# Kernel tuning notes

Measured on AMD Instinct MI355X. Metric: run time of the kernel, lower is better.

The kernel has to match this reference:

```python
import jax, jax.numpy as jnp
import numpy as np

HID = 512      # hidden_dim
SEQ = 784      # sequence length hard-coded via make_discrete_HiPPO_nojit(hidden, 784)
BATCH = 1024
OUT = 10


def make_discrete_hippo(N, L):
    # HiPPO-LegS continuous matrices (standard construction)
    n = np.arange(N, dtype=np.float64)
    P = np.sqrt(1.0 + 2.0 * n)
    A = P[:, None] * P[None, :]
    A = -(np.tril(A) - np.diag(n))          # (N, N)
    B = np.sqrt(2.0 * n + 1.0).reshape(N, 1)  # (N, 1)
    # bilinear (Tustin) discretization with step = 1/L
    step = 1.0 / L
    I = np.eye(N)
    BL = np.linalg.inv(I - (step / 2.0) * A)
    Ad = BL @ (I + (step / 2.0) * A)
    Bd = (BL * step) @ B
    return jnp.asarray(Ad, jnp.float32), jnp.asarray(Bd[:, 0], jnp.float32)


def setup_inputs() -> dict:
    key = jax.random.key(0)
    k1, k2, k3, k4 = jax.random.split(key, 4)
    x = jax.random.normal(k1, (BATCH, SEQ), jnp.float32)
    # xavier-uniform C params (flax nn.initializers.xavier_uniform)
    a0 = float(np.sqrt(6.0 / (1 + HID)))
    a1 = float(np.sqrt(6.0 / (HID + HID)))
    C0 = jax.random.uniform(k2, (1, HID), jnp.float32, -a0, a0)
    C1 = jax.random.uniform(k3, (HID, HID), jnp.float32, -a1, a1)
    # final Dense(output_dim): lecun_normal kernel, zero bias
    W = jax.random.normal(k4, (HID, OUT), jnp.float32) / np.sqrt(HID)
    b = jnp.zeros((OUT,), jnp.float32)
    return {"x": x, "C0": C0, "C1": C1, "W": W, "b": b}


def _ssm_layer(A, Bvec, C, u):
    # u: (batch, seq) scalar input per step; returns ys: (seq, batch, d_out)
    def step(h, u_t):  # h: (batch, HID), u_t: (batch,)
        h_next = jnp.tanh(h @ A.T + u_t[:, None] * Bvec[None, :])
        y = h_next @ C.T
        return h_next, y
    h0 = jnp.zeros((u.shape[0], HID), u.dtype)
    _, ys = jax.lax.scan(step, h0, u.T)
    return ys


def reference(x, C0, C1, W, b):
    A, Bvec = make_discrete_hippo(HID, SEQ)  # trace-time constants
    y0 = _ssm_layer(A, Bvec, C0, x)[:, :, 0].T   # (batch, seq) scalar stream
    y1 = _ssm_layer(A, Bvec, C1, y0)             # (seq, batch, HID)
    logits = y1[-1] @ W + b                      # last timestep -> Dense
    return logits
```

## Files before the change

kernel.cpp:

```cpp
#include <hip/hip_runtime.h>
#include <math.h>

#define SEQL 784
#define HIDN 512
#define OUTD 10

typedef float v2 __attribute__((ext_vector_type(2)));

template<int CTRL, int RM>
__device__ __forceinline__ float dpp0(float v) {
    int r = __builtin_amdgcn_update_dpp(0, __builtin_bit_cast(int, v),
                                        CTRL, RM, 0xF, true);
    return __builtin_bit_cast(float, r);
}
__device__ __forceinline__ v2 sp(float v) { v2 r; r.x = v; r.y = v; return r; }
__device__ __forceinline__ v2 vfma(v2 a, v2 b, v2 c) {
    return __builtin_elementwise_fma(a, b, c);
}

__global__ __launch_bounds__(256) void compute_M(const float* __restrict__ C1,
                                                 const float* __restrict__ W,
                                                 float* __restrict__ M) {
    __shared__ float Ws[HIDN * OUTD];
    __shared__ float red[4][64][OUTD];
    const int lane = threadIdx.x & 63, w = threadIdx.x >> 6;
    const int i = blockIdx.x * 64 + lane;
    for (int idx = threadIdx.x; idx < HIDN * OUTD; idx += 256) Ws[idx] = W[idx];
    __syncthreads();
    float acc[OUTD];
#pragma unroll
    for (int o = 0; o < OUTD; ++o) acc[o] = 0.f;
    for (int j = w * 128; j < w * 128 + 128; ++j) {
        float cv = C1[j * HIDN + i];
#pragma unroll
        for (int o = 0; o < OUTD; ++o) acc[o] = fmaf(cv, Ws[j * OUTD + o], acc[o]);
    }
#pragma unroll
    for (int o = 0; o < OUTD; ++o) red[w][lane][o] = acc[o];
    __syncthreads();
    if (w == 0) {
#pragma unroll
        for (int o = 0; o < OUTD; ++o)
            M[i * OUTD + o] = (red[0][lane][o] + red[1][lane][o]) +
                              (red[2][lane][o] + red[3][lane][o]);
    }
}

__global__ __launch_bounds__(256, 1) void ssm_main(const float* __restrict__ x,
                                                   const float* __restrict__ C0,
                                                   const float* __restrict__ Mmat,
                                                   const float* __restrict__ bias,
                                                   float* __restrict__ out) {
    const int tid = threadIdx.x;
    const int wave = tid >> 6;
    const int lane = tid & 63;
    const int row = blockIdx.x * 4 + wave;

    __shared__ __align__(16) float xs[4][SEQL + 8];

    const float DEL = 1.0f / 784.0f;
    {
        const float4* __restrict__ xv =
            (const float4*)(x + (size_t)blockIdx.x * 4 * SEQL);
#pragma unroll
        for (int it = 0; it < 4; ++it) {
            int idx = tid + it * 256;
            if (idx < SEQL) {
                float4 v = xv[idx];
                int r = idx / (SEQL / 4);
                int c = (idx % (SEQL / 4)) * 4;
                float4 w;
                w.x = DEL * v.x; w.y = DEL * v.y;
                w.z = DEL * v.z; w.w = DEL * v.w;
                *(float4*)&xs[r][c] = w;
            }
        }
    }
    if (tid < 32) xs[tid >> 3][SEQL + (tid & 7)] = 0.f;
    __syncthreads();

    const double cd = 1.0 / 1568.0;
    const double F = 2.0 * 1.4426950408889634;
    float P[8], Ps[8], a_[8], G2[8], mE2[8], FT[8], C0d[8], K_[8];
    double apD = 0.0, bpD = 1.0;
    double Aprod = 1.0;
#pragma unroll
    for (int j = 0; j < 8; ++j) {
        int i = lane * 8 + j;
        double Pd = sqrt(1.0 + 2.0 * (double)i);
        double dd = 1.0 + cd * (double)(i + 1);
        double fd = 1.0 / dd;
        double ad = (1.0 - cd * (double)i) * fd;
        double mEd = -cd * Pd * fd;
        double ed = Pd * mEd;
        double Gd = (1.0 - cd * (double)(i + 1)) * fd;
        apD = ad * apD + ed;
        bpD = ad * bpD;
        P[j]   = (float)Pd;
        Ps[j]  = (float)(Pd / F);
        a_[j]  = (float)ad;
        G2[j]  = (float)(F * Gd);
        mE2[j] = (float)(F * mEd);
        FT[j]  = (float)(F * Pd * fd);
        K_[j]  = (float)(F * mEd * Aprod);
        Aprod *= ad;
        C0d[j] = DEL * C0[i];
    }
    float ac[6], bc[6];
    {
        double al = apD, be = bpD;
        int rl = lane & 15;
#pragma unroll
        for (int L = 0; L < 4; ++L) {
            int d = 1 << L;
            ac[L] = (float)al; bc[L] = (float)be;
            double pa = __shfl_up(al, d, 64);
            double pb = __shfl_up(be, d, 64);
            if (rl >= d) { al += be * pa; be *= pb; }
        }
        ac[4] = (float)al; bc[4] = (float)be;
        {
            int src = (lane & 32) + 15;
            double pa = __shfl(al, src, 64);
            double pb = __shfl(be, src, 64);
            if (lane & 16) { al += be * pa; be *= pb; }
        }
        ac[5] = (float)al; bc[5] = (float)be;
        {
            double pa = __shfl(al, 31, 64);
            double pb = __shfl(be, 31, 64);
            if (lane >= 32) { al += be * pa; be *= pb; }
        }
    }

    v2 h[8];
#pragma unroll
    for (int j = 0; j < 8; ++j) h[j] = sp(0.f);

    float y0_d1 = 0.f, y0_d2 = 0.f;
    float u1 = xs[wave][0];

#pragma unroll 4
    for (int k = 0; k < SEQL + 2; ++k) {
        float u_next = xs[wave][k + 1];
        v2 du; du.x = u1; du.y = y0_d2;

        v2 w8[8];
        v2 r = sp(0.f), s = sp(0.f);
#pragma unroll
        for (int j = 0; j < 8; ++j) {
            v2 hj = h[j];
            v2 in_ = vfma(sp(mE2[j]), r, sp(G2[j]) * hj);
            in_ = vfma(sp(FT[j]), du, in_);
            w8[j] = vfma(sp(mE2[j]), s, in_);
            v2 z = sp(Ps[j]) * in_;
            s = vfma(sp(a_[j]), s, z);
            r = vfma(sp(P[j]), hj, r);
        }

#define LVL(CTRL, RM, L) {                                                   \
        s.x = fmaf(dpp0<CTRL, RM>(s.x), bc[L], s.x);                         \
        s.x = fmaf(dpp0<CTRL, RM>(r.x), ac[L], s.x);                         \
        s.y = fmaf(dpp0<CTRL, RM>(s.y), bc[L], s.y);                         \
        s.y = fmaf(dpp0<CTRL, RM>(r.y), ac[L], s.y);                         \
        r.x += dpp0<CTRL, RM>(r.x);                                          \
        r.y += dpp0<CTRL, RM>(r.y); }
        LVL(0x111, 0xF, 0)
        LVL(0x112, 0xF, 1)
        LVL(0x114, 0xF, 2)
        LVL(0x118, 0xF, 3)
        LVL(0x142, 0xA, 4)
        LVL(0x143, 0xC, 5)
#undef LVL
        v2 ri, si;
        ri.x = dpp0<0x138, 0xF>(r.x);  ri.y = dpp0<0x138, 0xF>(r.y);
        si.x = dpp0<0x138, 0xF>(s.x);  si.y = dpp0<0x138, 0xF>(s.y);

        v2 yy[8], ep[8];
        float pm[8], rp[8];
        {
            v2 S0 = ri + si;
#pragma unroll
            for (int j = 0; j < 8; ++j)
                yy[j] = vfma(sp(K_[j]), S0, w8[j]);
        }
#pragma unroll
        for (int j = 0; j < 8; ++j) {
            ep[j].x = __builtin_amdgcn_exp2f(yy[j].x);
            ep[j].y = __builtin_amdgcn_exp2f(yy[j].y);
        }
#pragma unroll
        for (int j = 0; j < 8; ++j) {
            ep[j] = ep[j] + sp(1.f);
            pm[j] = ep[j].x * ep[j].y;
        }
#pragma unroll
        for (int j = 0; j < 8; ++j) rp[j] = __builtin_amdgcn_rcpf(pm[j]);
        float part = 0.f;
#pragma unroll
        for (int j = 0; j < 8; ++j) {
            float m2 = -2.f * rp[j];
            v2 sw; sw.x = ep[j].y; sw.y = ep[j].x;
            v2 hn = vfma(sw, sp(m2), sp(1.f));
            h[j] = hn;
            part = fmaf(C0d[j], hn.x, part);
        }
        part += dpp0<0x111, 0xF>(part);
        part += dpp0<0x112, 0xF>(part);
        part += dpp0<0x114, 0xF>(part);
        part += dpp0<0x118, 0xF>(part);
        part += dpp0<0x142, 0xA>(part);
        part += dpp0<0x143, 0xC>(part);
        y0_d2 = y0_d1;
        y0_d1 = __builtin_bit_cast(float,
                  __builtin_amdgcn_readlane(__builtin_bit_cast(int, part), 63));
        u1 = u_next;
    }

    float acc[OUTD];
#pragma unroll
    for (int o = 0; o < OUTD; ++o) acc[o] = 0.f;
#pragma unroll
    for (int j = 0; j < 8; ++j) {
        float hv = h[j].y;
        int i = lane * 8 + j;
#pragma unroll
        for (int o = 0; o < OUTD; ++o)
            acc[o] = fmaf(hv, Mmat[i * OUTD + o], acc[o]);
    }
#pragma unroll
    for (int o = 0; o < OUTD; ++o) {
#pragma unroll
        for (int d = 32; d; d >>= 1) acc[o] += __shfl_xor(acc[o], d, 64);
    }
    if (lane == 0) {
#pragma unroll
        for (int o = 0; o < OUTD; ++o) out[row * OUTD + o] = acc[o] + bias[o];
    }
}

extern "C" void kernel_launch(void* const* d_in, const int* in_sizes, int n_in,
                              void* d_out, int out_size, void* d_ws, size_t ws_size,
                              hipStream_t stream) {
    const float* x  = (const float*)d_in[0];
    const float* C0 = (const float*)d_in[1];
    const float* C1 = (const float*)d_in[2];
    const float* W  = (const float*)d_in[3];
    const float* b  = (const float*)d_in[4];
    float* M = (float*)d_ws;

    compute_M<<<dim3(8), dim3(256), 0, stream>>>(C1, W, M);
    ssm_main<<<dim3(256), dim3(256), 0, stream>>>(x, C0, M, b, (float*)d_out);
}
```

Baseline: 411.8 us.

## Rescale in-lane scan and alternate lane roles to drop swizzle in tanh

The per-thread scan of s is rewritten as a prefix sum scaled by precomputed inverse cumulative products (Psp, PiL), which removes the dependent multiply chain through a_. The tanh/sigmoid is reformulated with a 0.5 fma so the x/y element swap disappears. To make that work, the two packed lanes swap their roles every other step through a templated do_step, with the loop unrolled by pairs. The rescaling by 1/Aprod may lose precision if the cumulative products get small.

```diff
diff --git a/kernel.cpp b/kernel.cpp
--- a/kernel.cpp
+++ b/kernel.cpp
@@ -44,6 +44,82 @@
             M[i * OUTD + o] = (red[0][lane][o] + red[1][lane][o]) +
                               (red[2][lane][o] + red[3][lane][o]);
     }
+}
+
+#define LVL(CTRL, RM, L) {                                                   \
+        s.x = fmaf(dpp0<CTRL, RM>(s.x), bc[L], s.x);                         \
+        s.x = fmaf(dpp0<CTRL, RM>(r.x), ac[L], s.x);                         \
+        s.y = fmaf(dpp0<CTRL, RM>(s.y), bc[L], s.y);                         \
+        s.y = fmaf(dpp0<CTRL, RM>(r.y), ac[L], s.y);                         \
+        r.x += dpp0<CTRL, RM>(r.x);                                          \
+        r.y += dpp0<CTRL, RM>(r.y); }
+
+template<int PSEL>
+static __device__ __forceinline__ float do_step(
+        v2 (&h)[8], v2 du,
+        const float (&P)[8], const float (&G2)[8], const float (&mE2)[8],
+        const float (&FT)[8], const float (&K_)[8], const float (&Psp)[8],
+        const float (&C0d)[8], float PiL,
+        const float (&ac)[6], const float (&bc)[6]) {
+    v2 w8[8];
+    v2 in0 = vfma(sp(FT[0]), du, sp(G2[0]) * h[0]);
+    w8[0] = in0;
+    v2 sg = sp(Psp[0]) * in0;
+    v2 r  = sp(P[0]) * h[0];
+#pragma unroll
+    for (int j = 1; j < 8; ++j) {
+        v2 hj = h[j];
+        v2 in_ = vfma(sp(mE2[j]), r, sp(G2[j]) * hj);
+        in_ = vfma(sp(FT[j]), du, in_);
+        w8[j] = vfma(sp(K_[j]), sg, in_);
+        sg = vfma(sp(Psp[j]), in_, sg);
+        r = vfma(sp(P[j]), hj, r);
+    }
+    v2 s = sp(PiL) * sg;
+
+    LVL(0x111, 0xF, 0)
+    LVL(0x112, 0xF, 1)
+    LVL(0x114, 0xF, 2)
+    LVL(0x118, 0xF, 3)
+    LVL(0x142, 0xA, 4)
+    LVL(0x143, 0xC, 5)
+    v2 ri, si;
+    ri.x = dpp0<0x138, 0xF>(r.x);  ri.y = dpp0<0x138, 0xF>(r.y);
+    si.x = dpp0<0x138, 0xF>(s.x);  si.y = dpp0<0x138, 0xF>(s.y);
+
+    v2 yy[8], ep[8];
+    float pm[8], rp[8];
+    {
+        v2 S0 = ri + si;
+#pragma unroll
+        for (int j = 0; j < 8; ++j)
+            yy[j] = vfma(sp(K_[j]), S0, w8[j]);
+    }
+#pragma unroll
+    for (int j = 0; j < 8; ++j) {
+        v2 E;
+        E.x = __builtin_amdgcn_exp2f(yy[j].x);
+        E.y = __builtin_amdgcn_exp2f(yy[j].y);
+        ep[j] = vfma(E, sp(0.5f), sp(0.5f));
+    }
+#pragma unroll
+    for (int j = 0; j < 8; ++j) pm[j] = ep[j].x * ep[j].y;
+#pragma unroll
+    for (int j = 0; j < 8; ++j) rp[j] = __builtin_amdgcn_rcpf(pm[j]);
+    float part = 0.f;
+#pragma unroll
+    for (int j = 0; j < 8; ++j) {
+        v2 hn = vfma(ep[j], sp(-rp[j]), sp(1.f));
+        h[j] = hn;
+        part = fmaf(C0d[j], PSEL ? hn.y : hn.x, part);
+    }
+    part += dpp0<0x111, 0xF>(part);
+    part += dpp0<0x112, 0xF>(part);
+    part += dpp0<0x114, 0xF>(part);
+    part += dpp0<0x118, 0xF>(part);
+    part += dpp0<0x142, 0xA>(part);
+    part += dpp0<0x143, 0xC>(part);
+    return part;
 }
 
 __global__ __launch_bounds__(256, 1) void ssm_main(const float* __restrict__ x,
@@ -81,7 +157,7 @@
 
     const double cd = 1.0 / 1568.0;
     const double F = 2.0 * 1.4426950408889634;
-    float P[8], Ps[8], a_[8], G2[8], mE2[8], FT[8], C0d[8], K_[8];
+    float P[8], G2[8], mE2[8], FT[8], C0d[8], K_[8], Psp[8], PiL;
     double apD = 0.0, bpD = 1.0;
     double Aprod = 1.0;
 #pragma unroll
@@ -97,15 +173,15 @@
         apD = ad * apD + ed;
         bpD = ad * bpD;
         P[j]   = (float)Pd;
-        Ps[j]  = (float)(Pd / F);
-        a_[j]  = (float)ad;
         G2[j]  = (float)(F * Gd);
         mE2[j] = (float)(F * mEd);
         FT[j]  = (float)(F * Pd * fd);
         K_[j]  = (float)(F * mEd * Aprod);
+        Psp[j] = (float)((Pd / F) / (Aprod * ad));
         Aprod *= ad;
         C0d[j] = DEL * C0[i];
     }
+    PiL = (float)Aprod;
     float ac[6], bc[6];
     {
         double al = apD, be = bpD;
@@ -140,81 +216,28 @@
     float y0_d1 = 0.f, y0_d2 = 0.f;
     float u1 = xs[wave][0];
 
-#pragma unroll 4
-    for (int k = 0; k < SEQL + 2; ++k) {
-        float u_next = xs[wave][k + 1];
-        v2 du; du.x = u1; du.y = y0_d2;
-
-        v2 w8[8];
-        v2 r = sp(0.f), s = sp(0.f);
-#pragma unroll
-        for (int j = 0; j < 8; ++j) {
-            v2 hj = h[j];
-            v2 in_ = vfma(sp(mE2[j]), r, sp(G2[j]) * hj);
-            in_ = vfma(sp(FT[j]), du, in_);
-            w8[j] = vfma(sp(mE2[j]), s, in_);
-            v2 z = sp(Ps[j]) * in_;
-            s = vfma(sp(a_[j]), s, z);
-            r = vfma(sp(P[j]), hj, r);
-        }
-
-#define LVL(CTRL, RM, L) {                                                   \
-        s.x = fmaf(dpp0<CTRL, RM>(s.x), bc[L], s.x);                         \
-        s.x = fmaf(dpp0<CTRL, RM>(r.x), ac[L], s.x);                         \
-        s.y = fmaf(dpp0<CTRL, RM>(s.y), bc[L], s.y);                         \
-        s.y = fmaf(dpp0<CTRL, RM>(r.y), ac[L], s.y);                         \
-        r.x += dpp0<CTRL, RM>(r.x);                                          \
-        r.y += dpp0<CTRL, RM>(r.y); }
-        LVL(0x111, 0xF, 0)
-        LVL(0x112, 0xF, 1)
-        LVL(0x114, 0xF, 2)
-        LVL(0x118, 0xF, 3)
-        LVL(0x142, 0xA, 4)
-        LVL(0x143, 0xC, 5)
-#undef LVL
-        v2 ri, si;
-        ri.x = dpp0<0x138, 0xF>(r.x);  ri.y = dpp0<0x138, 0xF>(r.y);
-        si.x = dpp0<0x138, 0xF>(s.x);  si.y = dpp0<0x138, 0xF>(s.y);
-
-        v2 yy[8], ep[8];
-        float pm[8], rp[8];
-        {
-            v2 S0 = ri + si;
-#pragma unroll
-            for (int j = 0; j < 8; ++j)
-                yy[j] = vfma(sp(K_[j]), S0, w8[j]);
-        }
-#pragma unroll
-        for (int j = 0; j < 8; ++j) {
-            ep[j].x = __builtin_amdgcn_exp2f(yy[j].x);
-            ep[j].y = __builtin_amdgcn_exp2f(yy[j].y);
-        }
-#pragma unroll
-        for (int j = 0; j < 8; ++j) {
-            ep[j] = ep[j] + sp(1.f);
-            pm[j] = ep[j].x * ep[j].y;
-        }
-#pragma unroll
-        for (int j = 0; j < 8; ++j) rp[j] = __builtin_amdgcn_rcpf(pm[j]);
-        float part = 0.f;
-#pragma unroll
-        for (int j = 0; j < 8; ++j) {
-            float m2 = -2.f * rp[j];
-            v2 sw; sw.x = ep[j].y; sw.y = ep[j].x;
-            v2 hn = vfma(sw, sp(m2), sp(1.f));
-            h[j] = hn;
-            part = fmaf(C0d[j], hn.x, part);
-        }
-        part += dpp0<0x111, 0xF>(part);
-        part += dpp0<0x112, 0xF>(part);
-        part += dpp0<0x114, 0xF>(part);
-        part += dpp0<0x118, 0xF>(part);
-        part += dpp0<0x142, 0xA>(part);
-        part += dpp0<0x143, 0xC>(part);
-        y0_d2 = y0_d1;
-        y0_d1 = __builtin_bit_cast(float,
-                  __builtin_amdgcn_readlane(__builtin_bit_cast(int, part), 63));
-        u1 = u_next;
+#pragma unroll 2
+    for (int k = 0; k < SEQL + 2; k += 2) {
+        {
+            float u_nx = xs[wave][k + 1];
+            v2 du; du.x = u1; du.y = y0_d2;
+            float part = do_step<1>(h, du, P, G2, mE2, FT, K_, Psp, C0d, PiL,
+                                    ac, bc);
+            y0_d2 = y0_d1;
+            y0_d1 = __builtin_bit_cast(float,
+                      __builtin_amdgcn_readlane(__builtin_bit_cast(int, part), 63));
+            u1 = u_nx;
+        }
+        {
+            float u_nx = xs[wave][k + 2];
+            v2 du; du.x = y0_d2; du.y = u1;
+            float part = do_step<0>(h, du, P, G2, mE2, FT, K_, Psp, C0d, PiL,
+                                    ac, bc);
+            y0_d2 = y0_d1;
+            y0_d1 = __builtin_bit_cast(float,
+                      __builtin_amdgcn_readlane(__builtin_bit_cast(int, part), 63));
+            u1 = u_nx;
+        }
     }
 
     float acc[OUTD];
```

Measured after the change: 411.3 us. No clear change (-0.1%).

## Split the two SSM layers across producer/consumer waves with a shared-memory ring

Applied to the files above, without the earlier changes.

Before this change, each wave ran both SSM layers in lockstep, packed into 2-wide float vectors. Now the block has 8 waves: four compute layer 0 and write y0 into a shared ring buffer, and four consume it eight steps later for layer 1. Block-wide barriers every 8 steps pipeline the two layers. The per-step maths is also reworked: the state is stored pre-scaled by G2, tanh uses a folded exp/rcp form, and the prefix-scan coefficients are rescaled to drop several FMAs. This removes the dual-lane packing cost and aims to double the waves in flight per block. In exchange it adds syncthreads overhead and raises per-CU register pressure under launch_bounds(512,2).

```diff
diff --git a/kernel.cpp b/kernel.cpp
--- a/kernel.cpp
+++ b/kernel.cpp
@@ -4,18 +4,12 @@
 #define SEQL 784
 #define HIDN 512
 #define OUTD 10
-
-typedef float v2 __attribute__((ext_vector_type(2)));
 
 template<int CTRL, int RM>
 __device__ __forceinline__ float dpp0(float v) {
     int r = __builtin_amdgcn_update_dpp(0, __builtin_bit_cast(int, v),
                                         CTRL, RM, 0xF, true);
     return __builtin_bit_cast(float, r);
-}
-__device__ __forceinline__ v2 sp(float v) { v2 r; r.x = v; r.y = v; return r; }
-__device__ __forceinline__ v2 vfma(v2 a, v2 b, v2 c) {
-    return __builtin_elementwise_fma(a, b, c);
 }
 
 __global__ __launch_bounds__(256) void compute_M(const float* __restrict__ C1,
@@ -46,7 +40,74 @@
     }
 }
 
-__global__ __launch_bounds__(256, 1) void ssm_main(const float* __restrict__ x,
+struct Consts {
+    float mE2[8], P2[8], G2[8], Psp[8], K_[8], C0d2[8];
+    float ac[6], bc[6];
+    float PiL;
+};
+
+template<bool PART>
+static __device__ __forceinline__ float sstep(float (&H)[8], float du,
+                                              const Consts& C) {
+    float w8[8];
+    float rt = -1568.0f * du;
+    float in0 = fmaf(C.mE2[0], rt, H[0]);
+    w8[0] = in0;
+    float g = C.Psp[0] * in0;
+    rt = fmaf(C.P2[0], H[0], rt);
+#pragma unroll
+    for (int j = 1; j < 8; ++j) {
+        float in_ = fmaf(C.mE2[j], rt, H[j]);
+        w8[j] = fmaf(C.K_[j], g, in_);
+        g = fmaf(C.Psp[j], in_, g);
+        rt = fmaf(C.P2[j], H[j], rt);
+    }
+    float r = fmaf(1568.0f, du, rt);
+    float s = C.PiL * g;
+
+#define LVLS(CTRL, RM, L) {                                                  \
+        s = fmaf(dpp0<CTRL, RM>(s), C.bc[L], s);                             \
+        s = fmaf(dpp0<CTRL, RM>(r), C.ac[L], s);                             \
+        r += dpp0<CTRL, RM>(r); }
+    LVLS(0x111, 0xF, 0)
+    LVLS(0x112, 0xF, 1)
+    LVLS(0x114, 0xF, 2)
+    LVLS(0x118, 0xF, 3)
+    LVLS(0x142, 0xA, 4)
+    LVLS(0x143, 0xC, 5)
+#undef LVLS
+    float t = r + s;
+    float S0 = dpp0<0x138, 0xF>(t);
+
+    float yy[8], ep[8];
+#pragma unroll
+    for (int j = 0; j < 8; ++j) yy[j] = fmaf(C.K_[j], S0, w8[j]);
+#pragma unroll
+    for (int j = 0; j < 8; ++j)
+        ep[j] = fmaf(__builtin_amdgcn_exp2f(yy[j]), 0.5f, 0.5f);
+#pragma unroll
+    for (int q = 0; q < 4; ++q) {
+        float rp = __builtin_amdgcn_rcpf(ep[2*q] * ep[2*q+1]);
+        float n0 = -C.G2[2*q]     * rp;
+        float n1 = -C.G2[2*q + 1] * rp;
+        H[2*q]     = fmaf(ep[2*q + 1], n0, C.G2[2*q]);
+        H[2*q + 1] = fmaf(ep[2*q],     n1, C.G2[2*q + 1]);
+    }
+    float part = 0.f;
+    if (PART) {
+#pragma unroll
+        for (int j = 0; j < 8; ++j) part = fmaf(C.C0d2[j], H[j], part);
+        part += dpp0<0x111, 0xF>(part);
+        part += dpp0<0x112, 0xF>(part);
+        part += dpp0<0x114, 0xF>(part);
+        part += dpp0<0x118, 0xF>(part);
+        part += dpp0<0x142, 0xA>(part);
+        part += dpp0<0x143, 0xC>(part);
+    }
+    return part;
+}
+
+__global__ __launch_bounds__(512, 2) void ssm_main(const float* __restrict__ x,
                                                    const float* __restrict__ C0,
                                                    const float* __restrict__ Mmat,
                                                    const float* __restrict__ bias,
@@ -54,34 +115,36 @@
     const int tid = threadIdx.x;
     const int wave = tid >> 6;
     const int lane = tid & 63;
-    const int row = blockIdx.x * 4 + wave;
+    const int slot = wave & 3;
+    const int role = wave >> 2;
+    const int row = blockIdx.x * 4 + slot;
 
     __shared__ __align__(16) float xs[4][SEQL + 8];
+    __shared__ __align__(16) float ring[4][16];
 
     const float DEL = 1.0f / 784.0f;
     {
         const float4* __restrict__ xv =
             (const float4*)(x + (size_t)blockIdx.x * 4 * SEQL);
 #pragma unroll
-        for (int it = 0; it < 4; ++it) {
-            int idx = tid + it * 256;
-            if (idx < SEQL) {
+        for (int it = 0; it < 2; ++it) {
+            int idx = tid + it * 512;
+            if (idx < 4 * (SEQL / 4)) {
                 float4 v = xv[idx];
-                int r = idx / (SEQL / 4);
-                int c = (idx % (SEQL / 4)) * 4;
+                int rr = idx / (SEQL / 4);
+                int cc = (idx % (SEQL / 4)) * 4;
                 float4 w;
                 w.x = DEL * v.x; w.y = DEL * v.y;
                 w.z = DEL * v.z; w.w = DEL * v.w;
-                *(float4*)&xs[r][c] = w;
+                *(float4*)&xs[rr][cc] = w;
             }
         }
     }
-    if (tid < 32) xs[tid >> 3][SEQL + (tid & 7)] = 0.f;
     __syncthreads();
 
     const double cd = 1.0 / 1568.0;
     const double F = 2.0 * 1.4426950408889634;
-    float P[8], Ps[8], a_[8], G2[8], mE2[8], FT[8], C0d[8], K_[8];
+    Consts C;
     double apD = 0.0, bpD = 1.0;
     double Aprod = 1.0;
 #pragma unroll
@@ -94,38 +157,37 @@
         double mEd = -cd * Pd * fd;
         double ed = Pd * mEd;
         double Gd = (1.0 - cd * (double)(i + 1)) * fd;
+        double G2d = F * Gd;
         apD = ad * apD + ed;
         bpD = ad * bpD;
-        P[j]   = (float)Pd;
-        Ps[j]  = (float)(Pd / F);
-        a_[j]  = (float)ad;
-        G2[j]  = (float)(F * Gd);
-        mE2[j] = (float)(F * mEd);
-        FT[j]  = (float)(F * Pd * fd);
-        K_[j]  = (float)(F * mEd * Aprod);
+        C.P2[j]  = (float)(Pd / G2d);
+        C.G2[j]  = (float)G2d;
+        C.mE2[j] = (float)(F * mEd);
+        C.K_[j]  = (float)(F * mEd * Aprod);
+        C.Psp[j] = (float)((Pd / F) / (Aprod * ad));
         Aprod *= ad;
-        C0d[j] = DEL * C0[i];
-    }
-    float ac[6], bc[6];
+        C.C0d2[j] = (float)((double)DEL * (double)C0[i] / G2d);
+    }
+    C.PiL = (float)Aprod;
     {
         double al = apD, be = bpD;
         int rl = lane & 15;
 #pragma unroll
         for (int L = 0; L < 4; ++L) {
             int d = 1 << L;
-            ac[L] = (float)al; bc[L] = (float)be;
+            C.ac[L] = (float)al; C.bc[L] = (float)be;
             double pa = __shfl_up(al, d, 64);
             double pb = __shfl_up(be, d, 64);
             if (rl >= d) { al += be * pa; be *= pb; }
         }
-        ac[4] = (float)al; bc[4] = (float)be;
+        C.ac[4] = (float)al; C.bc[4] = (float)be;
         {
             int src = (lane & 32) + 15;
             double pa = __shfl(al, src, 64);
             double pb = __shfl(be, src, 64);
             if (lane & 16) { al += be * pa; be *= pb; }
         }
-        ac[5] = (float)al; bc[5] = (float)be;
+        C.ac[5] = (float)al; C.bc[5] = (float)be;
         {
             double pa = __shfl(al, 31, 64);
             double pb = __shfl(be, 31, 64);
@@ -133,109 +195,60 @@
         }
     }
 
-    v2 h[8];
-#pragma unroll
-    for (int j = 0; j < 8; ++j) h[j] = sp(0.f);
-
-    float y0_d1 = 0.f, y0_d2 = 0.f;
-    float u1 = xs[wave][0];
-
-#pragma unroll 4
-    for (int k = 0; k < SEQL + 2; ++k) {
-        float u_next = xs[wave][k + 1];
-        v2 du; du.x = u1; du.y = y0_d2;
-
-        v2 w8[8];
-        v2 r = sp(0.f), s = sp(0.f);
+    float H[8];
+#pragma unroll
+    for (int j = 0; j < 8; ++j) H[j] = 0.f;
+
+    float* ringp = ring[slot];
+    const float* xrow = xs[slot];
+
+    for (int p = 0; p < 99; ++p) {
+        if (role == 0) {
+            if (p < 98) {
+                const float4* up = (const float4*)&xrow[p * 8];
+                float4 u0 = up[0], u1 = up[1];
+                float ub[8] = {u0.x, u0.y, u0.z, u0.w, u1.x, u1.y, u1.z, u1.w};
+                int base = (p * 8) & 15;
+#pragma unroll
+                for (int b = 0; b < 8; ++b) {
+                    float part = sstep<true>(H, ub[b], C);
+                    if (lane == 63) ringp[base + b] = part;
+                }
+            }
+        } else {
+            if (p >= 1) {
+                const float4* yp = (const float4*)&ringp[((p - 1) * 8) & 15];
+                float4 y0v = yp[0], y1v = yp[1];
+                float yb[8] = {y0v.x, y0v.y, y0v.z, y0v.w,
+                               y1v.x, y1v.y, y1v.z, y1v.w};
+#pragma unroll
+                for (int b = 0; b < 8; ++b) sstep<false>(H, yb[b], C);
+            }
+        }
+        __syncthreads();
+    }
+
+    if (role == 1) {
+        float acc[OUTD];
+#pragma unroll
+        for (int o = 0; o < OUTD; ++o) acc[o] = 0.f;
 #pragma unroll
         for (int j = 0; j < 8; ++j) {
-            v2 hj = h[j];
-            v2 in_ = vfma(sp(mE2[j]), r, sp(G2[j]) * hj);
-            in_ = vfma(sp(FT[j]), du, in_);
-            w8[j] = vfma(sp(mE2[j]), s, in_);
-            v2 z = sp(Ps[j]) * in_;
-            s = vfma(sp(a_[j]), s, z);
-            r = vfma(sp(P[j]), hj, r);
-        }
-
-#define LVL(CTRL, RM, L) {                                                   \
-        s.x = fmaf(dpp0<CTRL, RM>(s.x), bc[L], s.x);                         \
-        s.x = fmaf(dpp0<CTRL, RM>(r.x), ac[L], s.x);                         \
-        s.y = fmaf(dpp0<CTRL, RM>(s.y), bc[L], s.y);                         \
-        s.y = fmaf(dpp0<CTRL, RM>(r.y), ac[L], s.y);                         \
-        r.x += dpp0<CTRL, RM>(r.x);                                          \
-        r.y += dpp0<CTRL, RM>(r.y); }
-        LVL(0x111, 0xF, 0)
-        LVL(0x112, 0xF, 1)
-        LVL(0x114, 0xF, 2)
-        LVL(0x118, 0xF, 3)
-        LVL(0x142, 0xA, 4)
-        LVL(0x143, 0xC, 5)
-#undef LVL
-        v2 ri, si;
-        ri.x = dpp0<0x138, 0xF>(r.x);  ri.y = dpp0<0x138, 0xF>(r.y);
-        si.x = dpp0<0x138, 0xF>(s.x);  si.y = dpp0<0x138, 0xF>(s.y);
-
-        v2 yy[8], ep[8];
-        float pm[8], rp[8];
-        {
-            v2 S0 = ri + si;
-#pragma unroll
-            for (int j = 0; j < 8; ++j)
-                yy[j] = vfma(sp(K_[j]), S0, w8[j]);
-        }
-#pragma unroll
-        for (int j = 0; j < 8; ++j) {
-            ep[j].x = __builtin_amdgcn_exp2f(yy[j].x);
-            ep[j].y = __builtin_amdgcn_exp2f(yy[j].y);
-        }
-#pragma unroll
-        for (int j = 0; j < 8; ++j) {
-            ep[j] = ep[j] + sp(1.f);
-            pm[j] = ep[j].x * ep[j].y;
-        }
-#pragma unroll
-        for (int j = 0; j < 8; ++j) rp[j] = __builtin_amdgcn_rcpf(pm[j]);
-        float part = 0.f;
-#pragma unroll
-        for (int j = 0; j < 8; ++j) {
-            float m2 = -2.f * rp[j];
-            v2 sw; sw.x = ep[j].y; sw.y = ep[j].x;
-            v2 hn = vfma(sw, sp(m2), sp(1.f));
-            h[j] = hn;
-            part = fmaf(C0d[j], hn.x, part);
-        }
-        part += dpp0<0x111, 0xF>(part);
-        part += dpp0<0x112, 0xF>(part);
-        part += dpp0<0x114, 0xF>(part);
-        part += dpp0<0x118, 0xF>(part);
-        part += dpp0<0x142, 0xA>(part);
-        part += dpp0<0x143, 0xC>(part);
-        y0_d2 = y0_d1;
-        y0_d1 = __builtin_bit_cast(float,
-                  __builtin_amdgcn_readlane(__builtin_bit_cast(int, part), 63));
-        u1 = u_next;
-    }
-
-    float acc[OUTD];
-#pragma unroll
-    for (int o = 0; o < OUTD; ++o) acc[o] = 0.f;
-#pragma unroll
-    for (int j = 0; j < 8; ++j) {
-        float hv = h[j].y;
-        int i = lane * 8 + j;
-#pragma unroll
-        for (int o = 0; o < OUTD; ++o)
-            acc[o] = fmaf(hv, Mmat[i * OUTD + o], acc[o]);
-    }
-#pragma unroll
-    for (int o = 0; o < OUTD; ++o) {
-#pragma unroll
-        for (int d = 32; d; d >>= 1) acc[o] += __shfl_xor(acc[o], d, 64);
-    }
-    if (lane == 0) {
-#pragma unroll
-        for (int o = 0; o < OUTD; ++o) out[row * OUTD + o] = acc[o] + bias[o];
+            float hv = H[j] / C.G2[j];
+            int i = lane * 8 + j;
+#pragma unroll
+            for (int o = 0; o < OUTD; ++o)
+                acc[o] = fmaf(hv, Mmat[i * OUTD + o], acc[o]);
+        }
+#pragma unroll
+        for (int o = 0; o < OUTD; ++o) {
+#pragma unroll
+            for (int d = 32; d; d >>= 1) acc[o] += __shfl_xor(acc[o], d, 64);
+        }
+        if (lane == 0) {
+#pragma unroll
+            for (int o = 0; o < OUTD; ++o) out[row * OUTD + o] = acc[o] + bias[o];
+        }
     }
 }
 
@@ -250,5 +263,5 @@
     float* M = (float*)d_ws;
 
     compute_M<<<dim3(8), dim3(256), 0, stream>>>(C1, W, M);
-    ssm_main<<<dim3(256), dim3(256), 0, stream>>>(x, C0, M, b, (float*)d_out);
-}
+    ssm_main<<<dim3(256), dim3(512), 0, stream>>>(x, C0, M, b, (float*)d_out);
+}
```

Result: slower. 428.6 us (+4.1%).
